# Kernel optimization log

Measured on AMD Instinct MI355X. Metric: run time of the kernel, lower is better.

Reference implementation:

```python
import jax, jax.numpy as jnp
import numpy as np

B, HN, N1, DIM = 4096, 16, 192, 256
EPS = 1e-5


def _xavier(key, fan_out, fan_in):
    limit = np.sqrt(6.0 / (fan_in + fan_out)).astype(np.float32)
    return jax.random.uniform(key, (fan_out, fan_in), jnp.float32, -limit, limit)


def setup_inputs() -> dict:
    key = jax.random.key(0)
    k_rgb, k_tir, k_idx, k_w1, k_w2 = jax.random.split(key, 5)
    attn_rgb_weight = jax.random.uniform(k_rgb, (B, HN, N1), jnp.float32)
    attn_tir_weight = jax.random.uniform(k_tir, (B, HN, N1), jnp.float32)
    # unique, sorted indices per batch into [0, DIM) (scatter with duplicate
    # indices is nondeterministic in torch, so we keep them unique)
    idx = jax.vmap(lambda k: jax.random.permutation(k, DIM)[:N1])(
        jax.random.split(k_idx, B))
    global_index_s = jnp.sort(idx, axis=-1).astype(jnp.int32)
    return {
        "attn_rgb_weight": attn_rgb_weight,
        "attn_tir_weight": attn_tir_weight,
        "global_index_s": global_index_s,
        "ln_g": jnp.ones((2 * DIM,), jnp.float32),
        "ln_b": jnp.zeros((2 * DIM,), jnp.float32),
        "W1": _xavier(k_w1, DIM, 2 * DIM),   # Linear(512 -> 256), torch (out,in)
        "b1": jnp.zeros((DIM,), jnp.float32),
        "W2": _xavier(k_w2, 2 * DIM, DIM),   # Linear(256 -> 512)
        "b2": jnp.zeros((2 * DIM,), jnp.float32),
    }


def reference(attn_rgb_weight, attn_tir_weight, global_index_s,
              ln_g, ln_b, W1, b1, W2, b2):
    b, hn, n1 = attn_rgb_weight.shape
    idx = global_index_s[:, None, :]                     # [B, 1, N1]
    bi = jnp.arange(b)[:, None, None]                    # [B, 1, 1]
    hi = jnp.arange(hn)[None, :, None]                   # [1, hn, 1]
    # scatter sparse attention weights into dense [B, hn, DIM] buffers
    vex_rgb = jnp.zeros((b, hn, DIM), attn_rgb_weight.dtype)
    vex_rgb = vex_rgb.at[bi, hi, idx].set(attn_rgb_weight)
    vex_tir = jnp.zeros((b, hn, DIM), attn_tir_weight.dtype)
    vex_tir = vex_tir.at[bi, hi, idx].set(attn_tir_weight)
    vex = jnp.concatenate([vex_rgb, vex_tir], axis=-1)   # [B, hn, 2*DIM]
    # LayerNorm(2*DIM) -> Linear -> ReLU -> Linear -> Sigmoid
    mu = jnp.mean(vex, axis=-1, keepdims=True)
    var = jnp.mean(jnp.square(vex - mu), axis=-1, keepdims=True)
    x = (vex - mu) * jax.lax.rsqrt(var + EPS) * ln_g + ln_b
    h = jax.nn.relu(jnp.einsum('bhe,de->bhd', x, W1) + b1)
    o = jax.nn.sigmoid(jnp.einsum('bhd,ed->bhe', h, W2) + b2)  # [B, hn, 2*DIM]
    # gather back via index
    idx_full = jnp.broadcast_to(idx, (b, hn, n1))
    out_rgb = jnp.take_along_axis(o[:, :, :DIM], idx_full, axis=-1)
    out_tir = jnp.take_along_axis(o[:, :, DIM:], idx_full, axis=-1)
    return (out_rgb, out_tir)
```

## Files before the change

kernel.cpp:

```cpp
#include <hip/hip_runtime.h>
#include <stdint.h>

#define NJ 192
#define OUT_HALF 12582912

#define XS 520
#define HS 264
#define OSD 516

#define SLOTB  16384
#define H_OFF  33280
#define STAT_OFF 67072
#define ARENA  67584

typedef __attribute__((ext_vector_type(4))) float    f32x4;
typedef __attribute__((ext_vector_type(2))) float    f32x2;
typedef __attribute__((ext_vector_type(4))) int      i32x4;
typedef __attribute__((ext_vector_type(4))) uint32_t u32x4;
typedef __attribute__((ext_vector_type(8))) short    bf16x8;

__device__ float g_u1[256];
__device__ float g_v1[256];

__device__ __forceinline__ uint32_t cvt_pk_bf16(float lo, float hi) {
    uint32_t r;
    asm("v_cvt_pk_bf16_f32 %0, %1, %2" : "=v"(r) : "v"(lo), "v"(hi));
    return r;
}
__device__ __forceinline__ void gload16(const void* g, void* l) {
    __builtin_amdgcn_global_load_lds(
        (const __attribute__((address_space(1))) uint32_t*)g,
        (__attribute__((address_space(3))) uint32_t*)l, 16, 0, 0);
}

__global__ __launch_bounds__(256)
void pack_weights(const float* __restrict__ W1, const float* __restrict__ W2,
                  const float* __restrict__ ln_g, const float* __restrict__ ln_b,
                  const float* __restrict__ b1, short* __restrict__ ws) {
    if (blockIdx.x == 128) {
        int d = threadIdx.x;
        float u = b1[d], v = 0.f;
        const float* wr = W1 + d * 512;
        for (int e = 0; e < 512; e += 4) {
            f32x4 w4 = *(const f32x4*)(wr + e);
            f32x4 g4 = *(const f32x4*)(ln_g + e);
            f32x4 l4 = *(const f32x4*)(ln_b + e);
            #pragma unroll
            for (int t = 0; t < 4; ++t) { v += w4[t] * g4[t]; u += w4[t] * l4[t]; }
        }
        g_u1[d] = u; g_v1[d] = v;
        return;
    }
    int id = blockIdx.x * 256 + threadIdx.x;
    if (id < 16384) {
        int u8 = id >> 9, w = id & 511;
        int c = u8 >> 1, h = u8 & 1;
        int t2 = w >> 6, lane = w & 63;
        int nt = 2 * t2 + h;
        int row = nt * 16 + (lane & 15);
        int k0 = c * 16 + ((lane >> 4) << 2);
        f32x4 a  = *(const f32x4*)(W1 + row * 512 + k0);
        f32x4 b  = *(const f32x4*)(W1 + row * 512 + 256 + k0);
        f32x4 ga = *(const f32x4*)(ln_g + k0);
        f32x4 gb = *(const f32x4*)(ln_g + 256 + k0);
        u32x4 o;
        #pragma unroll
        for (int t = 0; t < 4; ++t) o[t] = cvt_pk_bf16(a[t] * ga[t], b[t] * gb[t]);
        *(u32x4*)(ws + id * 8) = o;
    } else {
        int id2 = id - 16384;
        int u16 = id2 >> 10, w = id2 & 1023;
        int c = u16 >> 1, h = u16 & 1;
        int t2 = w >> 6, lane = w & 63;
        int nt = 2 * t2 + h;
        int rp = nt * 16 + (lane & 15);
        int orow = (rp >> 1) + (rp & 1) * 256;
        int k0 = c * 32 + ((lane >> 4) << 3);
        f32x4 a = *(const f32x4*)(W2 + orow * 256 + k0);
        f32x4 b = *(const f32x4*)(W2 + orow * 256 + k0 + 4);
        u32x4 o;
        o[0] = cvt_pk_bf16(a[0], a[1]);
        o[1] = cvt_pk_bf16(a[2], a[3]);
        o[2] = cvt_pk_bf16(b[0], b[1]);
        o[3] = cvt_pk_bf16(b[2], b[3]);
        *(u32x4*)(ws + 131072 + id2 * 8) = o;
    }
}

__global__ __launch_bounds__(512, 4)
void fused_mlp(const float* __restrict__ rgb,
               const float* __restrict__ tir,
               const int*  __restrict__ gidx,
               const short* __restrict__ P1,
               const short* __restrict__ P2,
               const float* __restrict__ b2,
               float* __restrict__ out)
{
    __shared__ __attribute__((aligned(16))) char arena[ARENA];
    short* sX    = (short*)arena;
    short* sH    = (short*)(arena + H_OFF);
    float* sStat = (float*)(arena + STAT_OFF);
    float* sO    = (float*)arena;

    const int tid  = threadIdx.x;
    const int blk  = blockIdx.x;
    const int row0 = blk * 64;
    const int b0   = blk * 4;
    const int wave = tid >> 6;
    const int lane = tid & 63;
    const int lr   = lane & 15;
    const int quad = lane >> 4;
    const int mw   = wave & 3;
    const int nw   = wave >> 2;

    const char* P1b = (const char*)P1;
    const char* P2b = (const char*)P2;

    {
        uint32_t* xd = (uint32_t*)sX;
        #pragma unroll
        for (int i = 0; i < 8; ++i) {
            int u = i * 512 + tid;
            int r = u >> 6, g = u & 63;
            *(u32x4*)(xd + r * 260 + g * 4) = (u32x4){0u, 0u, 0u, 0u};
        }
    }
    __syncthreads();

    {
        int r = tid >> 3, sub = tid & 7;
        int j0 = sub * 24;
        uint32_t* xdw = (uint32_t*)(sX + r * XS);
        const int*   gp = gidx + (b0 + (r >> 4)) * NJ + j0;
        const float* rp = rgb + (row0 + r) * NJ + j0;
        const float* tp = tir + (row0 + r) * NJ + j0;
        float s = 0.f, ss = 0.f;
        #pragma unroll
        for (int q = 0; q < 6; ++q) {
            i32x4 iv = *(const i32x4*)(gp + q * 4);
            f32x4 vr = *(const f32x4*)(rp + q * 4);
            f32x4 vt = *(const f32x4*)(tp + q * 4);
            #pragma unroll
            for (int e = 0; e < 4; ++e) {
                s  += vr[e] + vt[e];
                ss += vr[e] * vr[e] + vt[e] * vt[e];
                xdw[iv[e]] = cvt_pk_bf16(vr[e], vt[e]);
            }
        }
        s  += __shfl_xor(s, 1, 8);  ss += __shfl_xor(ss, 1, 8);
        s  += __shfl_xor(s, 2, 8);  ss += __shfl_xor(ss, 2, 8);
        s  += __shfl_xor(s, 4, 8);  ss += __shfl_xor(ss, 4, 8);
        float mu  = s * (1.f / 512.f);
        float var = ss * (1.f / 512.f) - mu * mu;
        float rs  = rsqrtf(var + 1e-5f);
        if (sub == 0) { sStat[2 * r] = rs; sStat[2 * r + 1] = mu * rs; }
    }
    __syncthreads();

    bf16x8 a1[16];
    {
        const short* xr = sX + (mw * 16 + lr) * XS + quad * 8;
        #pragma unroll
        for (int c = 0; c < 16; ++c) a1[c] = *(const bf16x8*)(xr + c * 32);
    }
    __syncthreads();

    gload16(P1b + 0 * 8192 + tid * 16, arena + 0       + wave * 1024);
    gload16(P1b + 1 * 8192 + tid * 16, arena + SLOTB   + wave * 1024);
    __syncthreads();

    f32x4 acc1[8];
    #pragma unroll
    for (int i = 0; i < 8; ++i) acc1[i] = (f32x4){0.f, 0.f, 0.f, 0.f};

    const short* wb = (const short*)arena + lane * 8;

    #pragma unroll
    for (int j = 0; j < 32; ++j) {
        const int c = j >> 1, h = j & 1;
        bf16x8 w0 = *(const bf16x8*)(wb + (j & 1) * 8192 + (nw * 4 + 0) * 512);
        bf16x8 w1 = *(const bf16x8*)(wb + (j & 1) * 8192 + (nw * 4 + 1) * 512);
        bf16x8 w2 = *(const bf16x8*)(wb + (j & 1) * 8192 + (nw * 4 + 2) * 512);
        bf16x8 w3 = *(const bf16x8*)(wb + (j & 1) * 8192 + (nw * 4 + 3) * 512);
        __syncthreads();
        if (j <= 29) {
            gload16(P1b + (j + 2) * 8192 + tid * 16,
                    arena + (j & 1) * SLOTB + wave * 1024);
        } else {
            const int u = j - 30;
            gload16(P2b + u * 16384 + tid * 16,
                    arena + u * SLOTB + wave * 1024);
            gload16(P2b + u * 16384 + 8192 + tid * 16,
                    arena + u * SLOTB + 8192 + wave * 1024);
        }
        acc1[0 + h] = __builtin_amdgcn_mfma_f32_16x16x32_bf16(a1[c], w0, acc1[0 + h], 0, 0, 0);
        acc1[2 + h] = __builtin_amdgcn_mfma_f32_16x16x32_bf16(a1[c], w1, acc1[2 + h], 0, 0, 0);
        acc1[4 + h] = __builtin_amdgcn_mfma_f32_16x16x32_bf16(a1[c], w2, acc1[4 + h], 0, 0, 0);
        acc1[6 + h] = __builtin_amdgcn_mfma_f32_16x16x32_bf16(a1[c], w3, acc1[6 + h], 0, 0, 0);
    }

    {
        const int baserow = mw * 16 + quad * 4;
        float rsv[4], mrs[4];
        #pragma unroll
        for (int rr = 0; rr < 4; ++rr) {
            rsv[rr] = sStat[2 * (baserow + rr)];
            mrs[rr] = sStat[2 * (baserow + rr) + 1];
        }
        #pragma unroll
        for (int i = 0; i < 8; ++i) {
            int col = (nw * 8 + i) * 16 + lr;
            float u1c = g_u1[col], v1c = g_v1[col];
            #pragma unroll
            for (int rr = 0; rr < 4; ++rr) {
                float hh = rsv[rr] * acc1[i][rr] + (u1c - mrs[rr] * v1c);
                hh = fmaxf(hh, 0.f);
                sH[(baserow + rr) * HS + col] = (short)cvt_pk_bf16(hh, hh);
            }
        }
    }
    __syncthreads();

    f32x4 acc2[16];
    #pragma unroll
    for (int i = 0; i < 16; ++i) acc2[i] = (f32x4){0.f, 0.f, 0.f, 0.f};

    const short* hrow = sH + (mw * 16 + lr) * HS + quad * 8;

    #pragma unroll
    for (int j = 0; j < 16; ++j) {
        const int c = j >> 1, h = j & 1;
        bf16x8 a = *(const bf16x8*)(hrow + c * 32);
        bf16x8 w0 = *(const bf16x8*)(wb + (j & 1) * 8192 + (nw * 8 + 0) * 512);
        bf16x8 w1 = *(const bf16x8*)(wb + (j & 1) * 8192 + (nw * 8 + 1) * 512);
        bf16x8 w2 = *(const bf16x8*)(wb + (j & 1) * 8192 + (nw * 8 + 2) * 512);
        bf16x8 w3 = *(const bf16x8*)(wb + (j & 1) * 8192 + (nw * 8 + 3) * 512);
        bf16x8 w4 = *(const bf16x8*)(wb + (j & 1) * 8192 + (nw * 8 + 4) * 512);
        bf16x8 w5 = *(const bf16x8*)(wb + (j & 1) * 8192 + (nw * 8 + 5) * 512);
        bf16x8 w6 = *(const bf16x8*)(wb + (j & 1) * 8192 + (nw * 8 + 6) * 512);
        bf16x8 w7 = *(const bf16x8*)(wb + (j & 1) * 8192 + (nw * 8 + 7) * 512);
        __syncthreads();
        if (j <= 13) {
            gload16(P2b + (j + 2) * 16384 + tid * 16,
                    arena + (j & 1) * SLOTB + wave * 1024);
            gload16(P2b + (j + 2) * 16384 + 8192 + tid * 16,
                    arena + (j & 1) * SLOTB + 8192 + wave * 1024);
        }
        acc2[0  + h] = __builtin_amdgcn_mfma_f32_16x16x32_bf16(a, w0, acc2[0  + h], 0, 0, 0);
        acc2[2  + h] = __builtin_amdgcn_mfma_f32_16x16x32_bf16(a, w1, acc2[2  + h], 0, 0, 0);
        acc2[4  + h] = __builtin_amdgcn_mfma_f32_16x16x32_bf16(a, w2, acc2[4  + h], 0, 0, 0);
        acc2[6  + h] = __builtin_amdgcn_mfma_f32_16x16x32_bf16(a, w3, acc2[6  + h], 0, 0, 0);
        acc2[8  + h] = __builtin_amdgcn_mfma_f32_16x16x32_bf16(a, w4, acc2[8  + h], 0, 0, 0);
        acc2[10 + h] = __builtin_amdgcn_mfma_f32_16x16x32_bf16(a, w5, acc2[10 + h], 0, 0, 0);
        acc2[12 + h] = __builtin_amdgcn_mfma_f32_16x16x32_bf16(a, w6, acc2[12 + h], 0, 0, 0);
        acc2[14 + h] = __builtin_amdgcn_mfma_f32_16x16x32_bf16(a, w7, acc2[14 + h], 0, 0, 0);
    }

    const int prow = mw >> 1;
    const int baserow2 = (mw & 1) * 16 + quad * 4;

    #pragma unroll
    for (int p = 0; p < 2; ++p) {
        if (prow == p) {
            #pragma unroll
            for (int i = 0; i < 16; ++i) {
                int colp = (nw * 16 + i) * 16 + lr;
                float b2v = b2[(colp >> 1) + (colp & 1) * 256];
                #pragma unroll
                for (int rr = 0; rr < 4; ++rr) {
                    float x = acc2[i][rr] + b2v;
                    sO[(baserow2 + rr) * OSD + colp] = 1.f / (1.f + __expf(-x));
                }
            }
        }
        __syncthreads();
        #pragma unroll
        for (int it = 0; it < 3; ++it) {
            int q4 = (it * 512 + tid) * 4;
            int rl = q4 / NJ;
            int jj = q4 - rl * NJ;
            int r  = p * 32 + rl;
            i32x4 iv = *(const i32x4*)(gidx + (b0 + (r >> 4)) * NJ + jj);
            const float* orow = sO + rl * OSD;
            f32x4 vr, vt;
            #pragma unroll
            for (int e = 0; e < 4; ++e) {
                f32x2 pr = *(const f32x2*)(orow + 2 * iv[e]);
                vr[e] = pr[0]; vt[e] = pr[1];
            }
            *(f32x4*)&out[(row0 + r) * NJ + jj]            = vr;
            *(f32x4*)&out[OUT_HALF + (row0 + r) * NJ + jj] = vt;
        }
        if (p == 0) __syncthreads();
    }
}

extern "C" void kernel_launch(void* const* d_in, const int* in_sizes, int n_in,
                              void* d_out, int out_size, void* d_ws, size_t ws_size,
                              hipStream_t stream) {
    const float* rgb  = (const float*)d_in[0];
    const float* tir  = (const float*)d_in[1];
    const int*   gidx = (const int*)d_in[2];
    const float* ln_g = (const float*)d_in[3];
    const float* ln_b = (const float*)d_in[4];
    const float* W1   = (const float*)d_in[5];
    const float* b1   = (const float*)d_in[6];
    const float* W2   = (const float*)d_in[7];
    const float* b2   = (const float*)d_in[8];
    float* out = (float*)d_out;
    short* wsp = (short*)d_ws;

    pack_weights<<<129, 256, 0, stream>>>(W1, W2, ln_g, ln_b, b1, wsp);
    fused_mlp<<<1024, 512, 0, stream>>>(rgb, tir, gidx,
                                        wsp, wsp + 131072, b2, out);
}
```

Before: 270.0 us.

## Use 4-slot LDS weight pipeline with vmcnt waits and 32x32 MFMA for GEMM2

The double-buffered weight streaming is replaced by a 4-slot ring with prefetch depth 3. Each step uses explicit s_waitcnt vmcnt plus s_barrier instead of a full __syncthreads before each reload. GEMM2 is rewritten to use 32x32x16 MFMA tiles with a new packed W2 layout, and the hidden activations are stored in LDS with an XOR swizzle instead of padding. This aims to hide global-load latency and cut LDS traffic and bank conflicts, at the cost of more fragile manual wait counts and a different epilogue row mapping.

```diff
diff --git a/kernel.cpp b/kernel.cpp
--- a/kernel.cpp
+++ b/kernel.cpp
@@ -5,19 +5,18 @@
 #define OUT_HALF 12582912
 
 #define XS 520
-#define HS 264
 #define OSD 516
 
-#define SLOTB  16384
-#define H_OFF  33280
+#define H_BYTE 32768
 #define STAT_OFF 67072
 #define ARENA  67584
 
-typedef __attribute__((ext_vector_type(4))) float    f32x4;
-typedef __attribute__((ext_vector_type(2))) float    f32x2;
-typedef __attribute__((ext_vector_type(4))) int      i32x4;
-typedef __attribute__((ext_vector_type(4))) uint32_t u32x4;
-typedef __attribute__((ext_vector_type(8))) short    bf16x8;
+typedef __attribute__((ext_vector_type(4)))  float    f32x4;
+typedef __attribute__((ext_vector_type(16))) float    f32x16;
+typedef __attribute__((ext_vector_type(2)))  float    f32x2;
+typedef __attribute__((ext_vector_type(4)))  int      i32x4;
+typedef __attribute__((ext_vector_type(4)))  uint32_t u32x4;
+typedef __attribute__((ext_vector_type(8)))  short    bf16x8;
 
 __device__ float g_u1[256];
 __device__ float g_v1[256];
@@ -69,13 +68,14 @@
         *(u32x4*)(ws + id * 8) = o;
     } else {
         int id2 = id - 16384;
-        int u16 = id2 >> 10, w = id2 & 1023;
-        int c = u16 >> 1, h = u16 & 1;
-        int t2 = w >> 6, lane = w & 63;
-        int nt = 2 * t2 + h;
-        int rp = nt * 16 + (lane & 15);
-        int orow = (rp >> 1) + (rp & 1) * 256;
-        int k0 = c * 32 + ((lane >> 4) << 3);
+        int u = id2 >> 9;
+        int g = id2 & 511;
+        int f = g >> 6, lane = g & 63;
+        int k = u >> 1, h = u & 1;
+        int t = h * 8 + f;
+        int n = t * 32 + (lane & 31);
+        int orow = (n >> 1) + (n & 1) * 256;
+        int k0 = k * 16 + ((lane >> 5) << 3);
         f32x4 a = *(const f32x4*)(W2 + orow * 256 + k0);
         f32x4 b = *(const f32x4*)(W2 + orow * 256 + k0 + 4);
         u32x4 o;
@@ -98,7 +98,7 @@
 {
     __shared__ __attribute__((aligned(16))) char arena[ARENA];
     short* sX    = (short*)arena;
-    short* sH    = (short*)(arena + H_OFF);
+    short* sHsh  = (short*)(arena + H_BYTE);
     float* sStat = (float*)(arena + STAT_OFF);
     float* sO    = (float*)arena;
 
@@ -112,6 +112,8 @@
     const int quad = lane >> 4;
     const int mw   = wave & 3;
     const int nw   = wave >> 2;
+    const int mh   = wave >> 2;
+    const int nq   = wave & 3;
 
     const char* P1b = (const char*)P1;
     const char* P2b = (const char*)P2;
@@ -165,34 +167,33 @@
     }
     __syncthreads();
 
-    gload16(P1b + 0 * 8192 + tid * 16, arena + 0       + wave * 1024);
-    gload16(P1b + 1 * 8192 + tid * 16, arena + SLOTB   + wave * 1024);
-    __syncthreads();
+    gload16(P1b + 0 * 8192 + tid * 16, arena + 0 * 8192 + wave * 1024);
+    gload16(P1b + 1 * 8192 + tid * 16, arena + 1 * 8192 + wave * 1024);
+    gload16(P1b + 2 * 8192 + tid * 16, arena + 2 * 8192 + wave * 1024);
 
     f32x4 acc1[8];
     #pragma unroll
     for (int i = 0; i < 8; ++i) acc1[i] = (f32x4){0.f, 0.f, 0.f, 0.f};
-
-    const short* wb = (const short*)arena + lane * 8;
 
     #pragma unroll
     for (int j = 0; j < 32; ++j) {
         const int c = j >> 1, h = j & 1;
-        bf16x8 w0 = *(const bf16x8*)(wb + (j & 1) * 8192 + (nw * 4 + 0) * 512);
-        bf16x8 w1 = *(const bf16x8*)(wb + (j & 1) * 8192 + (nw * 4 + 1) * 512);
-        bf16x8 w2 = *(const bf16x8*)(wb + (j & 1) * 8192 + (nw * 4 + 2) * 512);
-        bf16x8 w3 = *(const bf16x8*)(wb + (j & 1) * 8192 + (nw * 4 + 3) * 512);
-        __syncthreads();
-        if (j <= 29) {
-            gload16(P1b + (j + 2) * 8192 + tid * 16,
-                    arena + (j & 1) * SLOTB + wave * 1024);
+        asm volatile("s_waitcnt vmcnt(2)" ::: "memory");
+        __builtin_amdgcn_s_barrier();
+        if (j <= 28) {
+            gload16(P1b + (j + 3) * 8192 + tid * 16,
+                    arena + ((j + 3) & 3) * 8192 + wave * 1024);
         } else {
-            const int u = j - 30;
-            gload16(P2b + u * 16384 + tid * 16,
-                    arena + u * SLOTB + wave * 1024);
-            gload16(P2b + u * 16384 + 8192 + tid * 16,
-                    arena + u * SLOTB + 8192 + wave * 1024);
-        }
+            gload16(P2b + (j - 29) * 8192 + tid * 16,
+                    arena + ((j + 3) & 3) * 8192 + wave * 1024);
+        }
+        const short* sb = (const short*)arena + ((j & 3) << 12);
+        bf16x8 w0 = *(const bf16x8*)(sb + (nw * 4 + 0) * 512 + lane * 8);
+        bf16x8 w1 = *(const bf16x8*)(sb + (nw * 4 + 1) * 512 + lane * 8);
+        bf16x8 w2 = *(const bf16x8*)(sb + (nw * 4 + 2) * 512 + lane * 8);
+        bf16x8 w3 = *(const bf16x8*)(sb + (nw * 4 + 3) * 512 + lane * 8);
+        asm volatile("s_waitcnt lgkmcnt(0)" ::: "memory");
+        __builtin_amdgcn_sched_barrier(0);
         acc1[0 + h] = __builtin_amdgcn_mfma_f32_16x16x32_bf16(a1[c], w0, acc1[0 + h], 0, 0, 0);
         acc1[2 + h] = __builtin_amdgcn_mfma_f32_16x16x32_bf16(a1[c], w1, acc1[2 + h], 0, 0, 0);
         acc1[4 + h] = __builtin_amdgcn_mfma_f32_16x16x32_bf16(a1[c], w2, acc1[4 + h], 0, 0, 0);
@@ -210,66 +211,65 @@
         #pragma unroll
         for (int i = 0; i < 8; ++i) {
             int col = (nw * 8 + i) * 16 + lr;
+            int blkc = col >> 3, within = col & 7;
             float u1c = g_u1[col], v1c = g_v1[col];
             #pragma unroll
             for (int rr = 0; rr < 4; ++rr) {
+                int r = baserow + rr;
                 float hh = rsv[rr] * acc1[i][rr] + (u1c - mrs[rr] * v1c);
                 hh = fmaxf(hh, 0.f);
-                sH[(baserow + rr) * HS + col] = (short)cvt_pk_bf16(hh, hh);
+                sHsh[r * 256 + ((blkc ^ (r & 31)) << 3) + within] = (short)cvt_pk_bf16(hh, hh);
             }
         }
     }
     __syncthreads();
 
-    f32x4 acc2[16];
-    #pragma unroll
-    for (int i = 0; i < 16; ++i) acc2[i] = (f32x4){0.f, 0.f, 0.f, 0.f};
-
-    const short* hrow = sH + (mw * 16 + lr) * HS + quad * 8;
-
-    #pragma unroll
-    for (int j = 0; j < 16; ++j) {
-        const int c = j >> 1, h = j & 1;
-        bf16x8 a = *(const bf16x8*)(hrow + c * 32);
-        bf16x8 w0 = *(const bf16x8*)(wb + (j & 1) * 8192 + (nw * 8 + 0) * 512);
-        bf16x8 w1 = *(const bf16x8*)(wb + (j & 1) * 8192 + (nw * 8 + 1) * 512);
-        bf16x8 w2 = *(const bf16x8*)(wb + (j & 1) * 8192 + (nw * 8 + 2) * 512);
-        bf16x8 w3 = *(const bf16x8*)(wb + (j & 1) * 8192 + (nw * 8 + 3) * 512);
-        bf16x8 w4 = *(const bf16x8*)(wb + (j & 1) * 8192 + (nw * 8 + 4) * 512);
-        bf16x8 w5 = *(const bf16x8*)(wb + (j & 1) * 8192 + (nw * 8 + 5) * 512);
-        bf16x8 w6 = *(const bf16x8*)(wb + (j & 1) * 8192 + (nw * 8 + 6) * 512);
-        bf16x8 w7 = *(const bf16x8*)(wb + (j & 1) * 8192 + (nw * 8 + 7) * 512);
-        __syncthreads();
-        if (j <= 13) {
-            gload16(P2b + (j + 2) * 16384 + tid * 16,
-                    arena + (j & 1) * SLOTB + wave * 1024);
-            gload16(P2b + (j + 2) * 16384 + 8192 + tid * 16,
-                    arena + (j & 1) * SLOTB + 8192 + wave * 1024);
-        }
-        acc2[0  + h] = __builtin_amdgcn_mfma_f32_16x16x32_bf16(a, w0, acc2[0  + h], 0, 0, 0);
-        acc2[2  + h] = __builtin_amdgcn_mfma_f32_16x16x32_bf16(a, w1, acc2[2  + h], 0, 0, 0);
-        acc2[4  + h] = __builtin_amdgcn_mfma_f32_16x16x32_bf16(a, w2, acc2[4  + h], 0, 0, 0);
-        acc2[6  + h] = __builtin_amdgcn_mfma_f32_16x16x32_bf16(a, w3, acc2[6  + h], 0, 0, 0);
-        acc2[8  + h] = __builtin_amdgcn_mfma_f32_16x16x32_bf16(a, w4, acc2[8  + h], 0, 0, 0);
-        acc2[10 + h] = __builtin_amdgcn_mfma_f32_16x16x32_bf16(a, w5, acc2[10 + h], 0, 0, 0);
-        acc2[12 + h] = __builtin_amdgcn_mfma_f32_16x16x32_bf16(a, w6, acc2[12 + h], 0, 0, 0);
-        acc2[14 + h] = __builtin_amdgcn_mfma_f32_16x16x32_bf16(a, w7, acc2[14 + h], 0, 0, 0);
-    }
-
-    const int prow = mw >> 1;
-    const int baserow2 = (mw & 1) * 16 + quad * 4;
+    f32x16 acc2[4];
+    #pragma unroll
+    for (int i = 0; i < 4; ++i)
+        #pragma unroll
+        for (int e = 0; e < 16; ++e) acc2[i][e] = 0.f;
+
+    bf16x8 a2frag;
+    #pragma unroll
+    for (int u = 0; u < 32; ++u) {
+        const int k = u >> 1, h = u & 1;
+        if (u <= 29)      asm volatile("s_waitcnt vmcnt(2)" ::: "memory");
+        else if (u == 30) asm volatile("s_waitcnt vmcnt(1)" ::: "memory");
+        else              asm volatile("s_waitcnt vmcnt(0)" ::: "memory");
+        __builtin_amdgcn_s_barrier();
+        if (u <= 28) {
+            gload16(P2b + (u + 3) * 8192 + tid * 16,
+                    arena + ((u + 3) & 3) * 8192 + wave * 1024);
+        }
+        if (h == 0) {
+            int r = mh * 32 + (lane & 31);
+            int blkc = (k * 2 + (lane >> 5)) ^ (r & 31);
+            a2frag = *(const bf16x8*)(sHsh + r * 256 + blkc * 8);
+        }
+        const short* sb = (const short*)arena + ((u & 3) << 12);
+        bf16x8 bf0 = *(const bf16x8*)(sb + (nq * 2 + 0) * 512 + lane * 8);
+        bf16x8 bf1 = *(const bf16x8*)(sb + (nq * 2 + 1) * 512 + lane * 8);
+        asm volatile("s_waitcnt lgkmcnt(0)" ::: "memory");
+        __builtin_amdgcn_sched_barrier(0);
+        acc2[h * 2 + 0] = __builtin_amdgcn_mfma_f32_32x32x16_bf16(a2frag, bf0, acc2[h * 2 + 0], 0, 0, 0);
+        acc2[h * 2 + 1] = __builtin_amdgcn_mfma_f32_32x32x16_bf16(a2frag, bf1, acc2[h * 2 + 1], 0, 0, 0);
+    }
+    __syncthreads();
 
     #pragma unroll
     for (int p = 0; p < 2; ++p) {
-        if (prow == p) {
-            #pragma unroll
-            for (int i = 0; i < 16; ++i) {
-                int colp = (nw * 16 + i) * 16 + lr;
+        if (mh == p) {
+            #pragma unroll
+            for (int ai = 0; ai < 4; ++ai) {
+                int t = (ai >> 1) * 8 + nq * 2 + (ai & 1);
+                int colp = t * 32 + (lane & 31);
                 float b2v = b2[(colp >> 1) + (colp & 1) * 256];
                 #pragma unroll
-                for (int rr = 0; rr < 4; ++rr) {
-                    float x = acc2[i][rr] + b2v;
-                    sO[(baserow2 + rr) * OSD + colp] = 1.f / (1.f + __expf(-x));
+                for (int rg = 0; rg < 16; ++rg) {
+                    int lrow = (rg & 3) + 8 * (rg >> 2) + 4 * (lane >> 5);
+                    float x = acc2[ai][rg] + b2v;
+                    sO[lrow * OSD + colp] = 1.f / (1.f + __expf(-x));
                 }
             }
         }
```

Result: faster. 257.5 us (-4.6%).
